# Kernel tuning notes

Measured on AMD Instinct MI355X. Metric: run time of the kernel, lower is better.

Reference implementation:

```python
import jax, jax.numpy as jnp
import numpy as np

NPG = 39      # nodes per graph, from (1+8+64+9)*(39+1)=3280 = lin1 in_features
NEG_SLOPE = 0.2


def gat_conv(x, src, dst, W, a_src, a_dst, b, n):
    """PyG GATConv, heads=1, self-loops already appended to (src, dst).
    x:[N,Fin] W:[Fin,Fout] a_src/a_dst:[Fout] b:[Fout] -> [N,Fout]"""
    h = x @ W                                        # [N,Fout]
    e = jax.nn.leaky_relu(h[src] @ a_src + h[dst] @ a_dst, NEG_SLOPE)  # [E]
    m = jax.lax.stop_gradient(jax.ops.segment_max(e, dst, num_segments=n))
    w = jnp.exp(e - m[dst])
    denom = jax.ops.segment_sum(w, dst, num_segments=n)
    alpha = w / (denom[dst] + 1e-16)                 # segment softmax per target node
    out = jax.ops.segment_sum(alpha[:, None] * h[src], dst, num_segments=n)
    return out + b


def setup_inputs() -> dict:
    key = jax.random.key(0)
    ks = jax.random.split(key, 20)
    B, DEG = 4096, 8
    N = B * NPG
    E = N * DEG
    x = jax.random.normal(ks[0], (N, 1), dtype=jnp.float32)
    # block-diagonal edges: each node emits DEG edges to random nodes in SAME graph
    src = jnp.repeat(jnp.arange(N, dtype=jnp.int64), DEG)
    offs = (src // NPG) * NPG
    dst = offs + jax.random.randint(ks[1], (E,), 0, NPG, dtype=jnp.int64)
    edge_index = jnp.stack([src, dst])
    batch_vec = jnp.repeat(jnp.arange(B, dtype=jnp.int64), NPG)

    def glorot(k, shape):
        fan = shape[0] + (shape[1] if len(shape) > 1 else 1)
        s = jnp.sqrt(6.0 / fan)
        return jax.random.uniform(k, shape, jnp.float32, -s, s)

    p = {
        'W1': glorot(ks[2], (1, 8)),   'a1s': glorot(ks[3], (8,)),  'a1d': glorot(ks[4], (8,)),  'b1': jnp.zeros((8,), jnp.float32),
        'W2': glorot(ks[5], (8, 64)),  'a2s': glorot(ks[6], (64,)), 'a2d': glorot(ks[7], (64,)), 'b2': jnp.zeros((64,), jnp.float32),
        'W3': glorot(ks[8], (64, 9)),  'a3s': glorot(ks[9], (9,)),  'a3d': glorot(ks[10], (9,)), 'b3': jnp.zeros((9,), jnp.float32),
        'lW1': glorot(ks[11], (3280, 5000)), 'lb1': jnp.zeros((5000,), jnp.float32),
        'lW2': glorot(ks[12], (5000, 1024)), 'lb2': jnp.zeros((1024,), jnp.float32),
        'lW3': glorot(ks[13], (1024, 9)),    'lb3': jnp.zeros((9,), jnp.float32),
    }
    return {'x': x, 'edge_index': edge_index, 'batch_vec': batch_vec, **p}


def reference(x, edge_index, batch_vec,
              W1, a1s, a1d, b1, W2, a2s, a2d, b2, W3, a3s, a3d, b3,
              lW1, lb1, lW2, lb2, lW3, lb3):
    N = x.shape[0]
    B = N // NPG
    loops = jnp.arange(N, dtype=edge_index.dtype)
    src = jnp.concatenate([edge_index[0], loops])   # GATConv add_self_loops=True
    dst = jnp.concatenate([edge_index[1], loops])

    res = x.reshape(B, -1)                                    # [B,39]
    out0 = jax.ops.segment_max(x, batch_vec, num_segments=B)  # [B,1]

    h1 = jax.nn.relu(gat_conv(x, src, dst, W1, a1s, a1d, b1, N))   # dropout = eval no-op
    res1 = h1.reshape(B, -1)                                   # [B,312]
    out1 = jax.ops.segment_max(h1, batch_vec, num_segments=B)

    h2 = jax.nn.relu(gat_conv(h1, src, dst, W2, a2s, a2d, b2, N))
    res2 = h2.reshape(B, -1)                                   # [B,2496]
    out2 = jax.ops.segment_max(h2, batch_vec, num_segments=B)

    h3 = jax.nn.relu(gat_conv(h2, src, dst, W3, a3s, a3d, b3, N))
    res3 = h3.reshape(B, -1)                                   # [B,351]
    out3 = jax.ops.segment_max(h3, batch_vec, num_segments=B)

    f = jnp.concatenate([res, res1, res2, res3, out0, out1, out2, out3], axis=1)  # [B,3280]
    f = jax.nn.relu(f @ lW1 + lb1)
    f = jax.nn.relu(f @ lW2 + lb2)
    return f @ lW3 + lb3                                       # [B,9]
```

## Files before the change

### kernel.cpp

```cpp
#include <hip/hip_runtime.h>
#include <hip/hip_bf16.h>
#include <hip/hip_fp16.h>
#include <stdint.h>


typedef float f32x4 __attribute__((ext_vector_type(4)));
typedef short bf16x8 __attribute__((ext_vector_type(8)));
typedef _Float16 f16x8 __attribute__((ext_vector_type(8)));

__device__ __forceinline__ unsigned fenc(float f) {
  int s = __float_as_int(f);
  return s < 0 ? ~(unsigned)s : ((unsigned)s | 0x80000000u);
}
__device__ __forceinline__ float fdec(unsigned u) {
  return (u & 0x80000000u) ? __int_as_float((int)(u & 0x7fffffffu))
                           : __int_as_float(~(int)u);
}

__device__ __forceinline__ void ldsbar() {
  asm volatile("s_waitcnt lgkmcnt(0)\n\ts_barrier" ::: "memory");
}


__global__ __launch_bounds__(128) void gnn_conv_seq(
    const float* __restrict__ x,
    const int* __restrict__ esrc, const int* __restrict__ edst,
    const float* __restrict__ W1, const float* __restrict__ a1s, const float* __restrict__ a1d, const float* __restrict__ b1,
    const float* __restrict__ W2, const float* __restrict__ a2s, const float* __restrict__ a2d, const float* __restrict__ b2,
    const float* __restrict__ W3, const float* __restrict__ a3s, const float* __restrict__ a3d, const float* __restrict__ b3,
    __hip_bfloat16* __restrict__ fA,
    const float* __restrict__ lW1, const float* __restrict__ lW2,
    short* __restrict__ W1T, short* __restrict__ W2T)
{
  __shared__ __align__(16) char smem[19840];
  const int tid = threadIdx.x;
  const int bid = blockIdx.x;

  if (bid >= 4096) {
    float (*t)[260] = (float(*)[260])smem;
    const int cid = bid - 4096;
    const float* W; short* WT; int ktile, ntile, K0, N0, KT;
    if (cid < 4160) { W = lW1; WT = W1T; ktile = cid % 208; ntile = cid / 208; K0 = 3280; N0 = 5000; KT = 52; }
    else { int c2 = cid - 4160; W = lW2; WT = W2T; ktile = c2 % 320; ntile = c2 / 320; K0 = 5000; N0 = 1024; KT = 80; }

    const int kb = ktile * 16, nb = ntile * 256;
    const int wv = tid >> 6, ln = tid & 63;
#pragma unroll
    for (int r = 0; r < 8; ++r) {
      int k = kb + wv * 8 + r;
      int n = nb + ln * 4;
      f32x4 v = (f32x4){0.f, 0.f, 0.f, 0.f};
      if (k < K0 && n < N0) v = *(const f32x4*)&W[(size_t)k * N0 + n];
      *(f32x4*)&t[wv * 8 + r][ln * 4] = v;
    }
    __syncthreads();
#pragma unroll
    for (int h = 0; h < 4; ++h) {
      int c = h * 128 + tid;
      int nl = c >> 1, kc = c & 1;
      int n = nb + nl, k = kb + kc * 8;
      union { bf16x8 v; __hip_bfloat16 b[8]; } z;
#pragma unroll
      for (int j = 0; j < 8; ++j) z.b[j] = __float2bfloat16(t[kc * 8 + j][nl]);
      int rt = n >> 7, mi = (n >> 4) & 7, lr = n & 15;
      int kt = k >> 6, kq = (k >> 5) & 1, lc = (k >> 3) & 3;
      size_t addr = ((((size_t)rt * KT) + kt) * 16 + mi * 2 + kq) * 512 + ((size_t)lr + 16 * lc) * 8;
      *(bf16x8*)&WT[addr] = z.v;
    }
    return;
  }

  float*    A     = (float*)   (smem);
  __half*   Hh2   = (__half*)  (smem + 6880);
  __half*   h1h   = (__half*)  (smem + 12512);
  float*    HfT   = (float*)   (smem + 13152);
  float*    sW3T  = (float*)   (smem + 14752);
  float*    xbuf  = (float*)   (smem + 17216);
  float*    a2buf = (float*)   (smem + 17376);
  float*    sarr  = (float*)   (smem + 17888);
  float*    darr  = (float*)   (smem + 18048);
  unsigned* umx   = (unsigned*)(smem + 18208);
  float*    a3sb  = (float*)   (smem + 18736);
  float*    a3db  = (float*)   (smem + 18784);
  float*    b3b   = (float*)   (smem + 18832);
  unsigned* cntP  = (unsigned*)(smem + 18880);

  const int g = bid, w = tid >> 6, f = tid & 63;
  const int dd3 = tid / 3, pp3 = tid - dd3 * 3;

  const int rt = g >> 7, mi = (g >> 4) & 7, lrow = g & 15;
  const size_t gbase = (size_t)rt * 52 * 8192 + (size_t)(mi * 2) * 512 + (size_t)lrow * 8;
#define COLADDR(c) (gbase + (size_t)((c) >> 6) * 8192 + (size_t)(((c) >> 5) & 1) * 512 \
                    + (size_t)(((c) >> 3) & 3) * 128 + ((c) & 7))

  auto denseEW = [&](const float* sv, const float* dv, float* sms) {
    if (tid < 117) {
      float dval = dv[dd3];
      float* Ar = &A[dd3 * 44];
      const unsigned* cr = &cntP[dd3 * 6];
      int s0 = pp3 * 13;
      float sum = 0.f;
#pragma unroll
      for (int k = 0; k < 13; ++k) {
        int s = s0 + k;
        float e = sv[s] + dval;
        e = (e > 0.f) ? e : 0.2f * e;
        unsigned c = (cr[s >> 3] >> (4 * (s & 7))) & 0xFu;
        float ex = __expf(e);
        float wv = c ? (float)c * ex : 0.f;
        Ar[s] = wv; sum += wv;
      }
      if (pp3 == 2) Ar[39] = 0.f;
      sms[tid] = sum;
    }
  };

  for (int i = tid; i < 576; i += 128) { int k = i / 9, f3 = i - 9 * k; sW3T[f3 * 68 + k] = W3[i]; }
  a2buf[tid] = (tid < 64) ? a2s[tid] : a2d[tid - 64];
  if (tid < 9) { a3sb[tid] = a3s[tid]; a3db[tid] = a3d[tid]; b3b[tid] = b3[tid]; }
  for (int i = tid; i < 132; i += 128) umx[i] = 0u;
  for (int i = tid; i < 234; i += 128) cntP[i] = 0u;
  if (tid < 40) xbuf[tid] = 0.f;

  float xv = 0.f;
  if (tid < 39) { xv = x[g * 39 + tid]; xbuf[tid] = xv; fA[COLADDR(tid)] = __float2bfloat16(xv); }

  float c_s = 0.f, c_d = 0.f;
  const float w1r = W1[tid & 7], b1r = b1[tid & 7];
#pragma unroll
  for (int ff = 0; ff < 8; ++ff) { float wv = W1[ff]; c_s += wv * a1s[ff]; c_d += wv * a1d[ff]; }
  const int eb = g * 312, nb0 = g * 39;
  ldsbar();

  if (tid < 39) atomicMax(&umx[0], fenc(xv));
#pragma unroll
  for (int it = 0; it < 3; ++it) {
    int e = it * 128 + tid;
    if (e < 351) {
      int ls, ld;
      if (e < 312) { ls = esrc[eb + e] - nb0; ld = edst[eb + e] - nb0; }
      else         { ls = e - 312; ld = ls; }
      atomicAdd(&cntP[ld * 6 + (ls >> 3)], 1u << (4 * (ls & 7)));
    }
  }
  if (f < 39) { if (w == 0) sarr[f] = xbuf[f] * c_s; else darr[f] = xbuf[f] * c_d; }
  ldsbar();

  denseEW(sarr, darr, &HfT[128]);
  ldsbar();
  if (tid < 39) {
    const float* Ar = &A[tid * 44];
    float q = 0.f;
#pragma unroll
    for (int c = 0; c < 10; ++c) {
      f32x4 a4 = *(const f32x4*)&Ar[c * 4];
      f32x4 x4 = *(const f32x4*)&xbuf[c * 4];
      q += a4.x * x4.x + a4.y * x4.y + a4.z * x4.z + a4.w * x4.w;
    }
    float inv = 1.f / (HfT[128 + 3 * tid] + HfT[129 + 3 * tid] + HfT[130 + 3 * tid] + 1e-16f);
    sarr[tid] = q * inv;
  }
  ldsbar();
#pragma unroll
  for (int it = 0; it < 3; ++it) {
    int slot = it * 128 + tid;
    if (slot < 312) {
      int i = slot >> 3, fi = slot & 7;
      float v = fmaxf(sarr[i] * w1r + b1r, 0.f);
      h1h[slot] = __float2half(v);
      fA[COLADDR(39 + slot)] = __float2bfloat16(v);
      atomicMax(&umx[1 + fi], fenc(v));
    }
  }
  ldsbar();

  float ht2r[40];
  {
    float w2k[8];
#pragma unroll
    for (int k = 0; k < 8; ++k) w2k[k] = W2[k * 64 + f];
#pragma unroll
    for (int i = 0; i < 39; ++i) {
      f16x8 hr = *(const f16x8*)&h1h[i * 8];
      float hv = 0.f;
#pragma unroll
      for (int k = 0; k < 8; ++k) hv += (float)hr[k] * w2k[k];
      ht2r[i] = hv;
    }
    ht2r[39] = 0.f;
#pragma unroll
    for (int i = 0; i < 39; ++i) {
      if ((i < 20) ? (w == 0) : (w == 1))
        Hh2[i * 72 + f] = __float2half(ht2r[i]);
    }
  }
  ldsbar();
  {
    int node = f;
    if (node < 39) {
      const float* ab = a2buf + (tid & 64);
      const __half* hr = &Hh2[node * 72];
      float s = 0.f;
#pragma unroll
      for (int c = 0; c < 8; ++c) {
        f16x8 hv = *(const f16x8*)&hr[c * 8];
        f32x4 a0 = *(const f32x4*)&ab[c * 8];
        f32x4 a1 = *(const f32x4*)&ab[c * 8 + 4];
        s += (float)hv[0] * a0.x + (float)hv[1] * a0.y + (float)hv[2] * a0.z + (float)hv[3] * a0.w
           + (float)hv[4] * a1.x + (float)hv[5] * a1.y + (float)hv[6] * a1.z + (float)hv[7] * a1.w;
      }
      if (tid < 64) sarr[node] = s; else darr[node] = s;
    }
  }
  ldsbar();
  denseEW(sarr, darr, &HfT[128]);
  ldsbar();
  {
    const float b2r = b2[f];
    for (int it = 0; it < 20; ++it) {
      int i = it * 2 + w;
      if (i < 39) {
        float inv = 1.f / (HfT[128 + 3 * i] + HfT[129 + 3 * i] + HfT[130 + 3 * i] + 1e-16f);
        const float* Ar = &A[i * 44];
        float acc = 0.f;
#pragma unroll
        for (int c = 0; c < 10; ++c) {
          f32x4 a4 = *(const f32x4*)&Ar[c * 4];
          acc += a4.x * ht2r[c * 4] + a4.y * ht2r[c * 4 + 1]
               + a4.z * ht2r[c * 4 + 2] + a4.w * ht2r[c * 4 + 3];
        }
        float v = fmaxf(acc * inv + b2r, 0.f);
        Hh2[i * 72 + f] = __float2half(v);
        fA[COLADDR(351 + i * 64 + f)] = __float2bfloat16(v);
        atomicMax(&umx[9 + f], fenc(v));
      }
    }
  }
  ldsbar();

  {
#pragma unroll
    for (int it = 0; it < 3; ++it) {
      int slot = it * 128 + tid;
      if (slot < 351) {
        int i = slot / 9, f3 = slot - 9 * i;
        const __half* hr = &Hh2[i * 72];
        const float* wr = &sW3T[f3 * 68];
        float acc = 0.f;
#pragma unroll
        for (int c = 0; c < 8; ++c) {
          f16x8 hv = *(const f16x8*)&hr[c * 8];
          f32x4 w0 = *(const f32x4*)&wr[c * 8];
          f32x4 w1 = *(const f32x4*)&wr[c * 8 + 4];
          acc += (float)hv[0] * w0.x + (float)hv[1] * w0.y + (float)hv[2] * w0.z + (float)hv[3] * w0.w
               + (float)hv[4] * w1.x + (float)hv[5] * w1.y + (float)hv[6] * w1.z + (float)hv[7] * w1.w;
        }
        HfT[f3 * 44 + i] = acc;
      }
    }
    if (tid < 9) HfT[tid * 44 + 39] = 0.f;
  }
  ldsbar();
  {
    int node = f;
    if (node < 39) {
      const float* av = (tid < 64) ? a3sb : a3db;
      float s = 0.f;
#pragma unroll
      for (int f3 = 0; f3 < 9; ++f3) s += HfT[f3 * 44 + node] * av[f3];
      if (tid < 64) sarr[node] = s; else darr[node] = s;
    }
  }
  ldsbar();
  denseEW(sarr, darr, &sW3T[128]);
  ldsbar();
#pragma unroll
  for (int it = 0; it < 3; ++it) {
    int slot = it * 128 + tid;
    if (slot < 351) {
      int i = slot / 9, f3 = slot - 9 * i;
      float inv = 1.f / (sW3T[128 + 3 * i] + sW3T[129 + 3 * i] + sW3T[130 + 3 * i] + 1e-16f);
      const float* Ar = &A[i * 44];
      const float* Hr = &HfT[f3 * 44];
      float acc = 0.f;
#pragma unroll
      for (int c = 0; c < 10; ++c) {
        f32x4 a4 = *(const f32x4*)&Ar[c * 4];
        f32x4 h4 = *(const f32x4*)&Hr[c * 4];
        acc += a4.x * h4.x + a4.y * h4.y + a4.z * h4.z + a4.w * h4.w;
      }
      float v = fmaxf(acc * inv + b3b[f3], 0.f);
      fA[COLADDR(2847 + slot)] = __float2bfloat16(v);
      atomicMax(&umx[73 + f3], fenc(v));
    }
  }
  ldsbar();

  if (tid < 130) {
    int c = 3198 + tid;
    float v = (tid < 82) ? fdec(umx[tid]) : 0.f;
    fA[COLADDR(c)] = __float2bfloat16(v);
  }
#undef COLADDR
}


__device__ __forceinline__ void gld_lds16(const void* gptr, void* l) {
  typedef const __attribute__((address_space(1))) unsigned int GU;
  typedef __attribute__((address_space(3))) unsigned int LU;
  __builtin_amdgcn_global_load_lds((GU*)gptr, (LU*)l, 16, 0, 0);
}

template<int MODE>
__global__ __launch_bounds__(256) void gemm_tiled(
    const short* __restrict__ A, const short* __restrict__ B,
    const float* __restrict__ bias, int Nreal,
    void* __restrict__ Cout, int Nn, int KT, int ktPerSplit, int outKT, int mt0)
{
  __shared__ __align__(16) short lA[8192];
  __shared__ __align__(16) short lB[8192];
  const int tid = threadIdx.x;
  const int w = tid >> 6, L = tid & 63;
  const int lrow = L & 15, lch = L >> 4;
  const int mt = blockIdx.y + mt0, nt = blockIdx.x;
  const int mw = (w >> 1) * 4, nw = (w & 1) * 4;
  const int kt0 = blockIdx.z * ktPerSplit, kt1 = kt0 + ktPerSplit;

  const short* Ab = A + ((size_t)mt * KT) * 8192 + (size_t)L * 8;
  const short* Bb = B + ((size_t)nt * KT) * 8192 + (size_t)L * 8;

  f32x4 acc[4][4] = {};

  for (int kt = kt0; kt < kt1; ++kt) {
    const short* Ak = Ab + (size_t)kt * 8192;
    const short* Bk = Bb + (size_t)kt * 8192;
#pragma unroll
    for (int j = 0; j < 4; ++j) {
      int st = w * 4 + j;
      gld_lds16(Ak + st * 512, &lA[st * 512]);
      gld_lds16(Bk + st * 512, &lB[st * 512]);
    }
    __syncthreads();
#pragma unroll
    for (int kk = 0; kk < 2; ++kk) {
      bf16x8 af[4], bfr[4];
#pragma unroll
      for (int i = 0; i < 4; ++i) {
        af[i]  = *(const bf16x8*)&lA[((mw + i) * 2 + kk) * 512 + L * 8];
        bfr[i] = *(const bf16x8*)&lB[((nw + i) * 2 + kk) * 512 + L * 8];
      }
#pragma unroll
      for (int i = 0; i < 4; ++i)
#pragma unroll
        for (int j = 0; j < 4; ++j)
          acc[i][j] = __builtin_amdgcn_mfma_f32_16x16x32_bf16(af[i], bfr[j], acc[i][j], 0, 0, 0);
    }
    __syncthreads();
  }

  if (MODE == 0) {
    __hip_bfloat16* C = (__hip_bfloat16*)Cout;
#pragma unroll
    for (int j = 0; j < 4; ++j) {
      int n = nt * 128 + (nw + j) * 16 + lrow;
      float bn = (n < Nreal) ? bias[n] : 0.f;
      int kt = n >> 6, kq = (n >> 5) & 1, lc2 = (n >> 3) & 3, j2 = n & 7;
#pragma unroll
      for (int i = 0; i < 4; ++i) {
        int mi = mw + i;
        size_t base = ((((size_t)mt * outKT + kt) * 16) + mi * 2 + kq) * 512
                      + (size_t)(lch * 4) * 8 + (size_t)lc2 * 128 + j2;
#pragma unroll
        for (int r = 0; r < 4; ++r)
          C[base + r * 8] = __float2bfloat16(fmaxf(acc[i][j][r] + bn, 0.f));
      }
    }
  } else {
    __half* P = (__half*)Cout + (size_t)blockIdx.z * 4096 * 1024;
#pragma unroll
    for (int j = 0; j < 4; ++j) {
      int n = nt * 128 + (nw + j) * 16 + lrow;
#pragma unroll
      for (int i = 0; i < 4; ++i)
#pragma unroll
        for (int r = 0; r < 4; ++r) {
          int m = mt * 128 + (mw + i) * 16 + lch * 4 + r;
          P[(size_t)m * Nn + n] = __float2half(acc[i][j][r]);
        }
    }
  }
}


__global__ __launch_bounds__(256) void gemm3_fused(
    const __half* __restrict__ P,
    const float* __restrict__ b2v,
    const float* __restrict__ W3,
    const float* __restrict__ b3v,
    float* __restrict__ out)
{
  __shared__ float sW3[9 * 1024];
  int tid = threadIdx.x;
  for (int i = tid; i < 9216; i += 256) { int k = i / 9, j = i - 9 * k; sW3[j * 1024 + k] = W3[i]; }
  __syncthreads();
  int row = blockIdx.x * 4 + (tid >> 6);
  int lane = tid & 63;
  const __half* p0 = P + (size_t)row * 1024;
  const size_t S = (size_t)4096 * 1024;
  float acc[9] = {0, 0, 0, 0, 0, 0, 0, 0, 0};
  for (int t = 0; t < 16; ++t) {
    int k = lane + 64 * t;
    float c = __half2float(p0[k]) + __half2float(p0[k + S])
            + __half2float(p0[k + 2 * S]) + __half2float(p0[k + 3 * S]) + b2v[k];
    c = fmaxf(c, 0.f);
#pragma unroll
    for (int j = 0; j < 9; ++j) acc[j] += c * sW3[j * 1024 + k];
  }
#pragma unroll
  for (int j = 0; j < 9; ++j) {
    float v = acc[j];
    v += __shfl_down(v, 32, 64);
    v += __shfl_down(v, 16, 64);
    v += __shfl_down(v, 8, 64);
    v += __shfl_down(v, 4, 64);
    v += __shfl_down(v, 2, 64);
    v += __shfl_down(v, 1, 64);
    if (lane == 0) out[(size_t)row * 9 + j] = v + b3v[j];
  }
}


extern "C" void kernel_launch(void* const* d_in, const int* in_sizes, int n_in,
                              void* d_out, int out_size, void* d_ws, size_t ws_size,
                              hipStream_t stream)
{
  const float* x   = (const float*)d_in[0];
  const int*   ei  = (const int*)d_in[1];
  const float* W1  = (const float*)d_in[3];
  const float* a1s = (const float*)d_in[4];
  const float* a1d = (const float*)d_in[5];
  const float* b1  = (const float*)d_in[6];
  const float* W2  = (const float*)d_in[7];
  const float* a2s = (const float*)d_in[8];
  const float* a2d = (const float*)d_in[9];
  const float* b2  = (const float*)d_in[10];
  const float* W3  = (const float*)d_in[11];
  const float* a3s = (const float*)d_in[12];
  const float* a3d = (const float*)d_in[13];
  const float* b3  = (const float*)d_in[14];
  const float* lW1 = (const float*)d_in[15];
  const float* lb1 = (const float*)d_in[16];
  const float* lW2 = (const float*)d_in[17];
  const float* lb2 = (const float*)d_in[18];
  const float* lW3 = (const float*)d_in[19];
  const float* lb3 = (const float*)d_in[20];

  const int E = 4096 * 39 * 8;
  const int* esrc = ei;
  const int* edst = ei + E;

  short* fA  = (short*)d_ws;
  short* W1T = fA  + (size_t)4096 * 3328;
  short* C1  = W1T + (size_t)5120 * 3328;
  short* W2T = C1  + (size_t)4096 * 5120;
  __half* P  = (__half*)d_ws;

  gnn_conv_seq<<<9536, 128, 0, stream>>>(x, esrc, edst,
                                         W1, a1s, a1d, b1, W2, a2s, a2d, b2, W3, a3s, a3d, b3,
                                         (__hip_bfloat16*)fA, lW1, lW2, W1T, W2T);
  gemm_tiled<0><<<dim3(40, 32, 1), 256, 0, stream>>>(fA, W1T, lb1, 5000, C1, 5120, 52, 52, 80, 0);
  gemm_tiled<1><<<dim3(8, 32, 4), 256, 0, stream>>>(C1, W2T, nullptr, 1024, P, 1024, 80, 20, 0, 0);
  gemm3_fused<<<1024, 256, 0, stream>>>(P, lb2, lW3, lb3, (float*)d_out);
}
```

Measured before the change: 434.1 us.

## Use 256x256 tile with 512 threads for second linear layer GEMM

The second GEMM (4096x1024x5120, split-K by 4) moves from a 128x128 tile kernel with 256 threads to a dedicated 256x256 tile kernel with 8 waves, each computing a 128x64 sub-tile. This doubles the reuse of each loaded A/B fragment and halves global/LDS traffic per MFMA. The cost is 64 KB of LDS per block, more accumulator registers, and only 256 blocks in the grid, which lowers occupancy and leaves load latency less hidden.

```diff
diff --git a/kernel.cpp b/kernel.cpp
--- a/kernel.cpp
+++ b/kernel.cpp
@@ -311,18 +311,17 @@
   __builtin_amdgcn_global_load_lds((GU*)gptr, (LU*)l, 16, 0, 0);
 }
 
-template<int MODE>
 __global__ __launch_bounds__(256) void gemm_tiled(
     const short* __restrict__ A, const short* __restrict__ B,
     const float* __restrict__ bias, int Nreal,
-    void* __restrict__ Cout, int Nn, int KT, int ktPerSplit, int outKT, int mt0)
+    void* __restrict__ Cout, int Nn, int KT, int ktPerSplit, int outKT)
 {
   __shared__ __align__(16) short lA[8192];
   __shared__ __align__(16) short lB[8192];
   const int tid = threadIdx.x;
   const int w = tid >> 6, L = tid & 63;
   const int lrow = L & 15, lch = L >> 4;
-  const int mt = blockIdx.y + mt0, nt = blockIdx.x;
+  const int mt = blockIdx.y, nt = blockIdx.x;
   const int mw = (w >> 1) * 4, nw = (w & 1) * 4;
   const int kt0 = blockIdx.z * ktPerSplit, kt1 = kt0 + ktPerSplit;
 
@@ -358,36 +357,84 @@
     __syncthreads();
   }
 
-  if (MODE == 0) {
-    __hip_bfloat16* C = (__hip_bfloat16*)Cout;
-#pragma unroll
-    for (int j = 0; j < 4; ++j) {
-      int n = nt * 128 + (nw + j) * 16 + lrow;
-      float bn = (n < Nreal) ? bias[n] : 0.f;
-      int kt = n >> 6, kq = (n >> 5) & 1, lc2 = (n >> 3) & 3, j2 = n & 7;
-#pragma unroll
-      for (int i = 0; i < 4; ++i) {
-        int mi = mw + i;
-        size_t base = ((((size_t)mt * outKT + kt) * 16) + mi * 2 + kq) * 512
-                      + (size_t)(lch * 4) * 8 + (size_t)lc2 * 128 + j2;
-#pragma unroll
-        for (int r = 0; r < 4; ++r)
-          C[base + r * 8] = __float2bfloat16(fmaxf(acc[i][j][r] + bn, 0.f));
-      }
-    }
-  } else {
-    __half* P = (__half*)Cout + (size_t)blockIdx.z * 4096 * 1024;
-#pragma unroll
-    for (int j = 0; j < 4; ++j) {
-      int n = nt * 128 + (nw + j) * 16 + lrow;
-#pragma unroll
-      for (int i = 0; i < 4; ++i)
-#pragma unroll
-        for (int r = 0; r < 4; ++r) {
-          int m = mt * 128 + (mw + i) * 16 + lch * 4 + r;
-          P[(size_t)m * Nn + n] = __float2half(acc[i][j][r]);
-        }
-    }
+  __hip_bfloat16* C = (__hip_bfloat16*)Cout;
+#pragma unroll
+  for (int j = 0; j < 4; ++j) {
+    int n = nt * 128 + (nw + j) * 16 + lrow;
+    float bn = (n < Nreal) ? bias[n] : 0.f;
+    int kt = n >> 6, kq = (n >> 5) & 1, lc2 = (n >> 3) & 3, j2 = n & 7;
+#pragma unroll
+    for (int i = 0; i < 4; ++i) {
+      int mi = mw + i;
+      size_t base = ((((size_t)mt * outKT + kt) * 16) + mi * 2 + kq) * 512
+                    + (size_t)(lch * 4) * 8 + (size_t)lc2 * 128 + j2;
+#pragma unroll
+      for (int r = 0; r < 4; ++r)
+        C[base + r * 8] = __float2bfloat16(fmaxf(acc[i][j][r] + bn, 0.f));
+    }
+  }
+}
+
+__global__ __launch_bounds__(512) void gemm2_256(
+    const short* __restrict__ A, const short* __restrict__ B,
+    __half* __restrict__ P)
+{
+  __shared__ __align__(16) short lA[16384];
+  __shared__ __align__(16) short lB[16384];
+  const int tid = threadIdx.x;
+  const int w = tid >> 6, L = tid & 63;
+  const int lrow = L & 15, lch = L >> 4;
+  const int wr = w >> 2, wc = w & 3;
+  const int nt = blockIdx.x, mt = blockIdx.y, zz = blockIdx.z;
+  const int kt0 = zz * 20, kt1 = kt0 + 20;
+
+  const short* A0 = A + ((size_t)(mt * 2) * 80) * 8192;
+  const short* A1 = A + ((size_t)(mt * 2 + 1) * 80) * 8192;
+  const short* B0 = B + ((size_t)(nt * 2) * 80) * 8192;
+  const short* B1 = B + ((size_t)(nt * 2 + 1) * 80) * 8192;
+
+  f32x4 acc[8][4] = {};
+
+  for (int kt = kt0; kt < kt1; ++kt) {
+    const size_t ko = (size_t)kt * 8192;
+#pragma unroll
+    for (int c = 0; c < 2; ++c) {
+      int off = (c * 512 + tid) * 8;
+      gld_lds16(A0 + ko + off, &lA[off]);
+      gld_lds16(A1 + ko + off, &lA[8192 + off]);
+      gld_lds16(B0 + ko + off, &lB[off]);
+      gld_lds16(B1 + ko + off, &lB[8192 + off]);
+    }
+    __syncthreads();
+#pragma unroll
+    for (int kk = 0; kk < 2; ++kk) {
+      bf16x8 af[8], bf[4];
+#pragma unroll
+      for (int i = 0; i < 8; ++i)
+        af[i] = *(const bf16x8*)&lA[wr * 8192 + (i * 2 + kk) * 512 + L * 8];
+#pragma unroll
+      for (int j = 0; j < 4; ++j)
+        bf[j] = *(const bf16x8*)&lB[(wc >> 1) * 8192 + (((wc & 1) * 4 + j) * 2 + kk) * 512 + L * 8];
+#pragma unroll
+      for (int i = 0; i < 8; ++i)
+#pragma unroll
+        for (int j = 0; j < 4; ++j)
+          acc[i][j] = __builtin_amdgcn_mfma_f32_16x16x32_bf16(af[i], bf[j], acc[i][j], 0, 0, 0);
+    }
+    __syncthreads();
+  }
+
+  __half* Pz = P + (size_t)zz * 4096 * 1024;
+#pragma unroll
+  for (int j = 0; j < 4; ++j) {
+    int n = nt * 256 + wc * 64 + j * 16 + lrow;
+#pragma unroll
+    for (int i = 0; i < 8; ++i)
+#pragma unroll
+      for (int r = 0; r < 4; ++r) {
+        int m = mt * 256 + wr * 128 + i * 16 + lch * 4 + r;
+        Pz[(size_t)m * 1024 + n] = __float2half(acc[i][j][r]);
+      }
   }
 }
 
@@ -468,7 +515,7 @@
   gnn_conv_seq<<<9536, 128, 0, stream>>>(x, esrc, edst,
                                          W1, a1s, a1d, b1, W2, a2s, a2d, b2, W3, a3s, a3d, b3,
                                          (__hip_bfloat16*)fA, lW1, lW2, W1T, W2T);
-  gemm_tiled<0><<<dim3(40, 32, 1), 256, 0, stream>>>(fA, W1T, lb1, 5000, C1, 5120, 52, 52, 80, 0);
-  gemm_tiled<1><<<dim3(8, 32, 4), 256, 0, stream>>>(C1, W2T, nullptr, 1024, P, 1024, 80, 20, 0, 0);
+  gemm_tiled<<<dim3(40, 32, 1), 256, 0, stream>>>(fA, W1T, lb1, 5000, C1, 5120, 52, 52, 80);
+  gemm2_256<<<dim3(4, 16, 4), 512, 0, stream>>>(C1, W2T, P);
   gemm3_fused<<<1024, 256, 0, stream>>>(P, lb2, lW3, lb3, (float*)d_out);
 }
```

New measurement: 450.7 us. +3.8%, slower.
